# Performance work log

Hardware: AMD Instinct MI355X
Metric: run time of the kernel (lower is better)

## Reference

```python
import jax, jax.numpy as jnp
import numpy as np

B, P, C = 32, 8732, 21
TOP_K = 200
CONF_THRESH = 0.01
NMS_THRESH = 0.45
VAR0, VAR1 = 0.1, 0.2  # VOC PRIOR_BOX VARIANCE


def setup_inputs() -> dict:
    key = jax.random.key(0)
    k1, k2, k3 = jax.random.split(key, 3)
    loc_data = jax.random.normal(k1, (B, P, 4), jnp.float32)
    conf_data = jax.random.uniform(k2, (B, P, C), jnp.float32)
    prior_data = jax.random.uniform(k3, (P, 4), jnp.float32)
    return {"loc_data": loc_data, "conf_data": conf_data, "prior_data": prior_data}


def _decode(loc, priors):
    # priors are (cx, cy, w, h); returns (x1, y1, x2, y2)
    cxcy = priors[:, :2] + loc[:, :2] * VAR0 * priors[:, 2:]
    wh = priors[:, 2:] * jnp.exp(loc[:, 2:] * VAR1)
    x1y1 = cxcy - wh * 0.5
    return jnp.concatenate([x1y1, x1y1 + wh], axis=1)  # [P,4]


def _nms_class(boxes, scores):
    # boxes [P,4], scores [P] -> [TOP_K,5] rows of (score, x1, y1, x2, y2)
    s = jnp.where(scores > CONF_THRESH, scores, -1.0)
    top_s, idx = jax.lax.top_k(s, TOP_K)          # descending scores
    b = boxes[idx]                                 # [K,4]
    valid = top_s > CONF_THRESH
    x1, y1, x2, y2 = b[:, 0], b[:, 1], b[:, 2], b[:, 3]
    area = (x2 - x1) * (y2 - y1)
    # pairwise intersection / IoU [K,K]
    xx1 = jnp.maximum(x1[:, None], x1[None, :])
    yy1 = jnp.maximum(y1[:, None], y1[None, :])
    xx2 = jnp.minimum(x2[:, None], x2[None, :])
    yy2 = jnp.minimum(y2[:, None], y2[None, :])
    inter = jnp.clip(xx2 - xx1, 0.0) * jnp.clip(yy2 - yy1, 0.0)
    union = area[:, None] + area[None, :] - inter
    iou = inter / union
    ar = jnp.arange(TOP_K)

    def step(carry, j):
        kept, suppressed = carry
        is_kept = valid[j] & ~suppressed[j]
        kept = kept.at[j].set(is_kept)
        suppressed = suppressed | (is_kept & (iou[j] > NMS_THRESH) & (ar > j))
        return (kept, suppressed), None

    (kept, _), _ = jax.lax.scan(
        step, (jnp.zeros(TOP_K, bool), jnp.zeros(TOP_K, bool)), ar)
    # compact kept rows to the front (matches output[i, cl, :count] = ...)
    pos = jnp.cumsum(kept) - 1
    safe = jnp.where(kept, pos, TOP_K)
    rows = jnp.concatenate([top_s[:, None], b], axis=1)  # [K,5]
    out = jnp.zeros((TOP_K + 1, 5), rows.dtype).at[safe].set(rows)[:TOP_K]
    return out


def reference(loc_data, conf_data, prior_data):
    def per_image(loc, conf):
        boxes = _decode(loc, prior_data)           # [P,4]
        return jax.vmap(lambda s: _nms_class(boxes, s), in_axes=1)(conf)  # [C,K,5]

    out = jax.vmap(per_image)(loc_data, conf_data)  # [B,C,K,5]
    return out.at[:, 0].set(0.0)  # class 0 (background) is skipped in original
```

## Files before the change

### kernel.cpp

```cpp
#include <hip/hip_runtime.h>
#include <stdint.h>

#define B_ 32
#define P_ 8732
#define PPAD 8736
#define C_ 21
#define TOPK 200
#define CONF_T 0.01f
#define NMS_T 0.45f
#define NCH2 35
#define NT 512
#define KV4 5

__device__ __forceinline__ uint32_t f2s(float f) {
    uint32_t u = __float_as_uint(f);
    return (u & 0x80000000u) ? ~u : (u | 0x80000000u);
}
__device__ __forceinline__ float s2f(uint32_t s) {
    uint32_t b = (s & 0x80000000u) ? (s & 0x7FFFFFFFu) : ~s;
    return __uint_as_float(b);
}

__global__ __launch_bounds__(256) void transpose_keys(const float* __restrict__ conf,
                                                      uint32_t* __restrict__ keys) {
    const int b = blockIdx.x / NCH2;
    const int ch = blockIdx.x % NCH2;
    const int p0 = ch * 256;
    const int n = min(256, P_ - p0);
    const int tid = threadIdx.x;
    __shared__ float tile[256 * C_];
    const float* src = conf + ((size_t)b * P_ + p0) * C_;
    const int tot = n * C_;
    for (int i = tid; i < tot; i += 256) tile[i] = src[i];
    __syncthreads();
    uint32_t* dst = keys + (size_t)b * C_ * PPAD + p0;
    if (tid < n) {
        #pragma unroll
        for (int c = 0; c < C_; ++c) {
            float v = tile[tid * C_ + c];
            v = (v > CONF_T) ? v : -1.0f;
            dst[(size_t)c * PPAD + tid] = f2s(v);
        }
    }
    if (ch == NCH2 - 1 && tid >= n && tid < n + (PPAD - P_)) {
        #pragma unroll
        for (int c = 0; c < C_; ++c) dst[(size_t)c * PPAD + tid] = 0u;
    }
}

template<bool RAW>
__global__ __launch_bounds__(NT, 6) void detect_kernel(
    const float* __restrict__ loc, const float* __restrict__ prior,
    const uint32_t* __restrict__ keys, const float* __restrict__ conf,
    float* __restrict__ out)
{
    const int task = blockIdx.x;
    const int b = task / C_;
    const int c = task % C_;
    const int tid = threadIdx.x;
    const int lane = tid & 63;
    float* outp = out + (size_t)task * TOPK * 5;

    if (c == 0) {
        for (int e = tid; e < TOPK * 5; e += NT) outp[e] = 0.0f;
        return;
    }

    __shared__ uint32_t hist[256];
    __shared__ uint32_t wtot[4];
    __shared__ uint64_t cand[256];
    __shared__ float4 bbox[TOPK];
    __shared__ float bar[TOPK], bs[TOPK];
    __shared__ unsigned long long msk[TOPK * 4];
    __shared__ unsigned long long vmask[4];
    __shared__ int order[TOPK];
    __shared__ int s_cnt, s_nk, s_flags;
    __shared__ uint32_t s_pref, s_want;

    uint4 kv[KV4];
    if (!RAW) {
        const uint4* kp = (const uint4*)(keys + (size_t)task * PPAD);
        #pragma unroll
        for (int r = 0; r < KV4; ++r) {
            int q = tid + r * NT;
            kv[r] = (q < PPAD / 4) ? kp[q] : make_uint4(0u, 0u, 0u, 0u);
        }
    } else {
        const float* sp = conf + (size_t)b * P_ * C_ + c;
        #pragma unroll
        for (int r = 0; r < KV4; ++r) {
            uint32_t uu[4];
            #pragma unroll
            for (int c4 = 0; c4 < 4; ++c4) {
                int p = (tid + r * NT) * 4 + c4;
                if (p < P_) {
                    float v = sp[(size_t)p * C_];
                    v = (v > CONF_T) ? v : -1.0f;
                    uu[c4] = f2s(v);
                } else uu[c4] = 0u;
            }
            kv[r] = make_uint4(uu[0], uu[1], uu[2], uu[3]);
        }
    }

    uint32_t pref = 0, want = TOPK;
    for (int level = 3; level >= 0; --level) {
        const int shift = level * 8;
        const uint32_t himask = (level == 3) ? 0u : (0xFFFFFFFFu << (shift + 8));
        if (tid < 256) hist[tid] = 0;
        __syncthreads();
        if (level == 3) {
            auto agg = [&](uint32_t u) {
                uint32_t bin = u >> 24;
                unsigned long long rem = __ballot(1);
                while (rem) {
                    int src = __ffsll(rem) - 1;
                    uint32_t bref = __shfl(bin, src);
                    unsigned long long same = __ballot(bin == bref) & rem;
                    if (lane == src) atomicAdd(&hist[bref], (uint32_t)__popcll(same));
                    rem &= ~same;
                }
            };
            #pragma unroll
            for (int r = 0; r < KV4; ++r) {
                agg(kv[r].x); agg(kv[r].y); agg(kv[r].z); agg(kv[r].w);
            }
        } else {
            auto one = [&](uint32_t u) {
                if ((u & himask) == pref) atomicAdd(&hist[(u >> shift) & 0xFFu], 1u);
            };
            #pragma unroll
            for (int r = 0; r < KV4; ++r) {
                one(kv[r].x); one(kv[r].y); one(kv[r].z); one(kv[r].w);
            }
        }
        __syncthreads();
        uint32_t h = 0, I = 0;
        if (tid < 256) {
            h = hist[tid];
            I = h;
            #pragma unroll
            for (int d = 1; d < 64; d <<= 1) {
                uint32_t v = __shfl_down(I, d);
                if (lane + d < 64) I += v;
            }
            if (lane == 0) wtot[tid >> 6] = I;
        }
        __syncthreads();
        if (tid < 256) {
            uint32_t off = 0;
            for (int w2 = (tid >> 6) + 1; w2 < 4; ++w2) off += wtot[w2];
            I += off;
            uint32_t E = I - h;
            if (I >= want && E < want) {
                s_pref = pref | ((uint32_t)tid << shift);
                s_want = want - E;
                s_flags = ((TOPK - want) + I <= 256) ? 1 : 0;
            }
        }
        __syncthreads();
        pref = s_pref; want = s_want;
        int done = s_flags;
        __syncthreads();
        if (done) break;
    }
    const uint32_t vthr = pref;

    if (tid == 0) s_cnt = 0;
    __syncthreads();
    #pragma unroll
    for (int r = 0; r < KV4; ++r) {
        const int pb = (tid + r * NT) * 4;
        uint32_t uu[4] = {kv[r].x, kv[r].y, kv[r].z, kv[r].w};
        #pragma unroll
        for (int c4 = 0; c4 < 4; ++c4) {
            uint32_t u = uu[c4];
            if (u >= vthr) {
                int pos = atomicAdd(&s_cnt, 1);
                if (pos < 256) cand[pos] = ((uint64_t)u << 32) | (uint32_t)(~(uint32_t)(pb + c4));
            }
        }
    }
    __syncthreads();
    if (tid < 256 && tid >= s_cnt) cand[tid] = 0ull;
    __syncthreads();

    uint64_t v = (tid < 256) ? cand[tid] : 0ull;
    for (int kk = 2; kk <= 256; kk <<= 1) {
        for (int j = kk >> 1; j > 0; j >>= 1) {
            if (j >= 64) {
                __syncthreads();
                if (tid < 256) cand[tid] = v;
                __syncthreads();
                if (tid < 256) {
                    uint64_t pv = cand[tid ^ j];
                    bool keepmax = (((tid & j) == 0) == ((tid & kk) == 0));
                    v = keepmax ? (v > pv ? v : pv) : (v < pv ? v : pv);
                }
            } else if (tid < 256) {
                uint64_t pv = __shfl_xor(v, j);
                bool keepmax = (((tid & j) == 0) == ((tid & kk) == 0));
                v = keepmax ? (v > pv ? v : pv) : (v < pv ? v : pv);
            }
        }
    }

    float my_sc = -1.0f;
    if (tid < TOPK) {
        uint32_t su = (uint32_t)(v >> 32);
        int p = (int)(~(uint32_t)v);
        my_sc = s2f(su);
        const float4 l4 = *(const float4*)(loc + ((size_t)b * P_ + p) * 4);
        const float4 pr = *(const float4*)(prior + (size_t)p * 4);
        float cx = __fadd_rn(pr.x, __fmul_rn(__fmul_rn(l4.x, 0.1f), pr.z));
        float cy = __fadd_rn(pr.y, __fmul_rn(__fmul_rn(l4.y, 0.1f), pr.w));
        float ew = (float)exp((double)__fmul_rn(l4.z, 0.2f));
        float eh = (float)exp((double)__fmul_rn(l4.w, 0.2f));
        float w  = __fmul_rn(pr.z, ew);
        float h  = __fmul_rn(pr.w, eh);
        float x1 = __fsub_rn(cx, __fmul_rn(w, 0.5f));
        float y1 = __fsub_rn(cy, __fmul_rn(h, 0.5f));
        float x2 = __fadd_rn(x1, w);
        float y2 = __fadd_rn(y1, h);
        bs[tid] = my_sc;
        bbox[tid] = make_float4(x1, y1, x2, y2);
        bar[tid] = __fmul_rn(__fsub_rn(x2, x1), __fsub_rn(y2, y1));
    }
    for (int i2 = tid; i2 < TOPK * 4; i2 += NT) msk[i2] = 0ull;
    {
        unsigned long long bm = __ballot(tid < TOPK && my_sc > CONF_T);
        if (lane == 0 && tid < 256) vmask[tid >> 6] = bm;
    }
    __syncthreads();

    if (tid < 500) {
        const int rp = tid / 5;
        const int s  = tid - rp * 5;
        #pragma unroll
        for (int pass = 0; pass < 2; ++pass) {
            const int j  = pass ? (199 - rp) : rp;
            const int i0 = pass ? (200 - rp + s) : (rp + 1 + s);
            const float4 bj = bbox[j];
            const float  aj = bar[j];
            for (int i = i0; i < TOPK; i += 5) {
                const float4 bi = bbox[i];
                float xx1 = fmaxf(bj.x, bi.x);
                float yy1 = fmaxf(bj.y, bi.y);
                float xx2 = fminf(bj.z, bi.z);
                float yy2 = fminf(bj.w, bi.w);
                float dx = fmaxf(__fsub_rn(xx2, xx1), 0.0f);
                float dy = fmaxf(__fsub_rn(yy2, yy1), 0.0f);
                float inter = __fmul_rn(dx, dy);
                if (inter > 0.0f) {
                    float uni = __fsub_rn(__fadd_rn(aj, bar[i]), inter);
                    float t45 = __fmul_rn(NMS_T, uni);
                    float mar = __fmul_rn(t45, 1e-6f);
                    bool sup;
                    if (inter > __fadd_rn(t45, mar)) sup = true;
                    else if (inter < __fsub_rn(t45, mar)) sup = false;
                    else sup = (inter / uni > NMS_T);
                    if (sup) atomicOr(&msk[j * 4 + (i >> 6)], 1ull << (i & 63));
                }
            }
        }
    }
    __syncthreads();

    if (tid < 64) {
        const int L = tid;
        unsigned long long s0 = 0, s1 = 0, s2 = 0, s3 = 0;
        const unsigned long long vm0 = vmask[0], vm1 = vmask[1],
                                 vm2 = vmask[2], vm3 = vmask[3];
        int nk = 0;
        #pragma unroll
        for (int w = 0; w < 4; ++w) {
            const int j = (w << 6) | L;
            unsigned long long r0 = 0, r1 = 0, r2 = 0, r3 = 0;
            if (j < TOPK) {
                const unsigned long long* mr = &msk[j * 4];
                r0 = mr[0]; r1 = mr[1]; r2 = mr[2]; r3 = mr[3];
            }
            const unsigned long long vw = (w == 0) ? vm0 : (w == 1) ? vm1
                                        : (w == 2) ? vm2 : vm3;
            const unsigned long long sw = (w == 0) ? s0 : (w == 1) ? s1
                                        : (w == 2) ? s2 : s3;
            unsigned long long alive = vw & ~sw;
            while (alive) {
                int jl = __ffsll(alive) - 1;
                if (L == 0) order[nk] = (w << 6) | jl;
                ++nk;
                s0 |= __shfl(r0, jl); s1 |= __shfl(r1, jl);
                s2 |= __shfl(r2, jl); s3 |= __shfl(r3, jl);
                const unsigned long long swn = (w == 0) ? s0 : (w == 1) ? s1
                                             : (w == 2) ? s2 : s3;
                alive &= ~swn;
                alive &= ~(1ull << jl);
            }
        }
        if (L == 0) s_nk = nk;
    }
    __syncthreads();

    const int nk = s_nk;
    for (int e = tid; e < TOPK * 5; e += NT) {
        int r = e / 5;
        int f = e - r * 5;
        float val = 0.0f;
        if (r < nk) {
            int j = order[r];
            float4 bb = bbox[j];
            val = (f == 0) ? bs[j] : (f == 1) ? bb.x : (f == 2) ? bb.y
                : (f == 3) ? bb.z : bb.w;
        }
        outp[e] = val;
    }
}

extern "C" void kernel_launch(void* const* d_in, const int* in_sizes, int n_in,
                              void* d_out, int out_size, void* d_ws, size_t ws_size,
                              hipStream_t stream) {
    const float* loc   = (const float*)d_in[0];
    const float* conf  = (const float*)d_in[1];
    const float* prior = (const float*)d_in[2];
    float* out = (float*)d_out;

    const size_t need = (size_t)B_ * C_ * PPAD * sizeof(uint32_t);
    if (ws_size >= need) {
        uint32_t* keys = (uint32_t*)d_ws;
        transpose_keys<<<B_ * NCH2, 256, 0, stream>>>(conf, keys);
        detect_kernel<false><<<B_ * C_, NT, 0, stream>>>(loc, prior, keys, conf, out);
    } else {
        detect_kernel<true><<<B_ * C_, NT, 0, stream>>>(loc, prior, nullptr, conf, out);
    }
}
```

Measured before the change: 138.4 us.

## Pack four NMS tasks per block and replace radix histogram with 2-bit threshold search

Each 1024-thread block now processes four (image, class) tasks with 256 threads each, instead of one task per 512-thread block. The 8-bit atomic-histogram radix select is replaced by a search that fixes two bits per round, counting keys above three candidate thresholds with per-thread compares and a packed wave reduction. The pairwise IoU work is redistributed over two lanes per row. This is meant to remove shared-memory atomic contention and idle threads, but it adds more select rounds, block-wide syncs shared across the four tasks, and more registers per thread (nine uint4 keys).

```diff
diff --git a/kernel.cpp b/kernel.cpp
--- a/kernel.cpp
+++ b/kernel.cpp
@@ -9,8 +9,12 @@
 #define CONF_T 0.01f
 #define NMS_T 0.45f
 #define NCH2 35
-#define NT 512
-#define KV4 5
+#define GT 4
+#define TT 256
+#define NTB (GT * TT)
+#define KV4 9
+#define NTASK (B_ * C_)
+#define NBLK (NTASK / GT)
 
 __device__ __forceinline__ uint32_t f2s(float f) {
     uint32_t u = __float_as_uint(f);
@@ -49,41 +53,38 @@
 }
 
 template<bool RAW>
-__global__ __launch_bounds__(NT, 6) void detect_kernel(
+__global__ __launch_bounds__(NTB, 4) void detect_kernel(
     const float* __restrict__ loc, const float* __restrict__ prior,
     const uint32_t* __restrict__ keys, const float* __restrict__ conf,
     float* __restrict__ out)
 {
-    const int task = blockIdx.x;
+    const int tid  = threadIdx.x;
+    const int sub  = tid >> 8;
+    const int tt   = tid & 255;
+    const int lane = tid & 63;
+    const int wv   = (tid >> 6) & 3;
+    const int task = blockIdx.x * GT + sub;
     const int b = task / C_;
     const int c = task % C_;
-    const int tid = threadIdx.x;
-    const int lane = tid & 63;
     float* outp = out + (size_t)task * TOPK * 5;
 
-    if (c == 0) {
-        for (int e = tid; e < TOPK * 5; e += NT) outp[e] = 0.0f;
-        return;
-    }
-
-    __shared__ uint32_t hist[256];
-    __shared__ uint32_t wtot[4];
-    __shared__ uint64_t cand[256];
-    __shared__ float4 bbox[TOPK];
-    __shared__ float bar[TOPK], bs[TOPK];
-    __shared__ unsigned long long msk[TOPK * 4];
-    __shared__ unsigned long long vmask[4];
-    __shared__ int order[TOPK];
-    __shared__ int s_cnt, s_nk, s_flags;
-    __shared__ uint32_t s_pref, s_want;
+    __shared__ uint64_t cand[GT][256];
+    __shared__ float4 bbox[GT][TOPK];
+    __shared__ float bar[GT][TOPK], bs[GT][TOPK];
+    __shared__ unsigned long long msk[GT][TOPK * 4];
+    __shared__ unsigned long long vmask[GT][4];
+    __shared__ int order[GT][TOPK];
+    __shared__ int s_cnt[GT], s_nk[GT];
+    __shared__ uint64_t warr[GT][4];
+    __shared__ uint32_t s_donemask;
 
     uint4 kv[KV4];
     if (!RAW) {
         const uint4* kp = (const uint4*)(keys + (size_t)task * PPAD);
         #pragma unroll
         for (int r = 0; r < KV4; ++r) {
-            int q = tid + r * NT;
-            kv[r] = (q < PPAD / 4) ? kp[q] : make_uint4(0u, 0u, 0u, 0u);
+            int q = tt + r * TT;
+            kv[r] = (c != 0 && q < PPAD / 4) ? kp[q] : make_uint4(0u, 0u, 0u, 0u);
         }
     } else {
         const float* sp = conf + (size_t)b * P_ * C_ + c;
@@ -91,122 +92,114 @@
         for (int r = 0; r < KV4; ++r) {
             uint32_t uu[4];
             #pragma unroll
-            for (int c4 = 0; c4 < 4; ++c4) {
-                int p = (tid + r * NT) * 4 + c4;
-                if (p < P_) {
+            for (int q = 0; q < 4; ++q) {
+                int p = (tt + r * TT) * 4 + q;
+                if (c != 0 && p < P_) {
                     float v = sp[(size_t)p * C_];
                     v = (v > CONF_T) ? v : -1.0f;
-                    uu[c4] = f2s(v);
-                } else uu[c4] = 0u;
+                    uu[q] = f2s(v);
+                } else uu[q] = 0u;
             }
             kv[r] = make_uint4(uu[0], uu[1], uu[2], uu[3]);
         }
     }
 
-    uint32_t pref = 0, want = TOPK;
-    for (int level = 3; level >= 0; --level) {
-        const int shift = level * 8;
-        const uint32_t himask = (level == 3) ? 0u : (0xFFFFFFFFu << (shift + 8));
-        if (tid < 256) hist[tid] = 0;
-        __syncthreads();
-        if (level == 3) {
-            auto agg = [&](uint32_t u) {
-                uint32_t bin = u >> 24;
-                unsigned long long rem = __ballot(1);
-                while (rem) {
-                    int src = __ffsll(rem) - 1;
-                    uint32_t bref = __shfl(bin, src);
-                    unsigned long long same = __ballot(bin == bref) & rem;
-                    if (lane == src) atomicAdd(&hist[bref], (uint32_t)__popcll(same));
-                    rem &= ~same;
-                }
-            };
+    if (tid == 0) s_donemask = 0;
+    if (tt == 0) s_cnt[sub] = 0;
+    __syncthreads();
+    if (c == 0 && tt == 0) atomicOr(&s_donemask, 1u << sub);
+    __syncthreads();
+
+    uint32_t pref = 0, cprev = KV4 * TT * 4;
+    int bp = 30;
+    bool done = (c == 0);
+    while (s_donemask != 0xFu) {
+        if (!done) {
+            const uint32_t tA = pref | (1u << bp);
+            const uint32_t tB = pref | (2u << bp);
+            const uint32_t tC = pref | (3u << bp);
+            uint32_t cA = 0, cB = 0, cC = 0;
             #pragma unroll
             for (int r = 0; r < KV4; ++r) {
-                agg(kv[r].x); agg(kv[r].y); agg(kv[r].z); agg(kv[r].w);
-            }
-        } else {
-            auto one = [&](uint32_t u) {
-                if ((u & himask) == pref) atomicAdd(&hist[(u >> shift) & 0xFFu], 1u);
-            };
+                const uint32_t uu[4] = {kv[r].x, kv[r].y, kv[r].z, kv[r].w};
+                #pragma unroll
+                for (int q = 0; q < 4; ++q) {
+                    const uint32_t u = uu[q];
+                    cA += (u >= tA); cB += (u >= tB); cC += (u >= tC);
+                }
+            }
+            unsigned long long pk = (unsigned long long)cA
+                                  | ((unsigned long long)cB << 21)
+                                  | ((unsigned long long)cC << 42);
             #pragma unroll
-            for (int r = 0; r < KV4; ++r) {
-                one(kv[r].x); one(kv[r].y); one(kv[r].z); one(kv[r].w);
-            }
+            for (int d = 1; d < 64; d <<= 1) pk += __shfl_down(pk, d);
+            if (lane == 0) warr[sub][wv] = pk;
         }
         __syncthreads();
-        uint32_t h = 0, I = 0;
-        if (tid < 256) {
-            h = hist[tid];
-            I = h;
+        if (!done) {
+            const unsigned long long tot = warr[sub][0] + warr[sub][1]
+                                         + warr[sub][2] + warr[sub][3];
+            const uint32_t M = (1u << 21) - 1;
+            const uint32_t cA = (uint32_t)tot & M;
+            const uint32_t cB = (uint32_t)(tot >> 21) & M;
+            const uint32_t cC = (uint32_t)(tot >> 42) & M;
+            uint32_t cNew;
+            if      (cC >= TOPK) { pref |= (3u << bp); cNew = cC; }
+            else if (cB >= TOPK) { pref |= (2u << bp); cNew = cB; }
+            else if (cA >= TOPK) { pref |= (1u << bp); cNew = cA; }
+            else                 { cNew = cprev; }
+            cprev = cNew;
+            bp -= 2;
+            if (cNew <= 256 || bp < 0) {
+                done = true;
+                if (tt == 0) atomicOr(&s_donemask, 1u << sub);
+            }
+        }
+        __syncthreads();
+    }
+    const uint32_t vthr = pref;
+
+    if (c != 0) {
+        #pragma unroll
+        for (int r = 0; r < KV4; ++r) {
+            const int pb = (tt + r * TT) * 4;
+            const uint32_t uu[4] = {kv[r].x, kv[r].y, kv[r].z, kv[r].w};
             #pragma unroll
-            for (int d = 1; d < 64; d <<= 1) {
-                uint32_t v = __shfl_down(I, d);
-                if (lane + d < 64) I += v;
-            }
-            if (lane == 0) wtot[tid >> 6] = I;
-        }
-        __syncthreads();
-        if (tid < 256) {
-            uint32_t off = 0;
-            for (int w2 = (tid >> 6) + 1; w2 < 4; ++w2) off += wtot[w2];
-            I += off;
-            uint32_t E = I - h;
-            if (I >= want && E < want) {
-                s_pref = pref | ((uint32_t)tid << shift);
-                s_want = want - E;
-                s_flags = ((TOPK - want) + I <= 256) ? 1 : 0;
-            }
-        }
-        __syncthreads();
-        pref = s_pref; want = s_want;
-        int done = s_flags;
-        __syncthreads();
-        if (done) break;
-    }
-    const uint32_t vthr = pref;
-
-    if (tid == 0) s_cnt = 0;
-    __syncthreads();
-    #pragma unroll
-    for (int r = 0; r < KV4; ++r) {
-        const int pb = (tid + r * NT) * 4;
-        uint32_t uu[4] = {kv[r].x, kv[r].y, kv[r].z, kv[r].w};
-        #pragma unroll
-        for (int c4 = 0; c4 < 4; ++c4) {
-            uint32_t u = uu[c4];
-            if (u >= vthr) {
-                int pos = atomicAdd(&s_cnt, 1);
-                if (pos < 256) cand[pos] = ((uint64_t)u << 32) | (uint32_t)(~(uint32_t)(pb + c4));
-            }
-        }
-    }
-    __syncthreads();
-    if (tid < 256 && tid >= s_cnt) cand[tid] = 0ull;
-    __syncthreads();
-
-    uint64_t v = (tid < 256) ? cand[tid] : 0ull;
+            for (int q = 0; q < 4; ++q) {
+                const uint32_t u = uu[q];
+                if (u >= vthr) {
+                    int pos = atomicAdd(&s_cnt[sub], 1);
+                    if (pos < 256) cand[sub][pos] = ((uint64_t)u << 32)
+                                                  | (uint32_t)(~(uint32_t)(pb + q));
+                }
+            }
+        }
+    }
+    __syncthreads();
+    if (tt >= s_cnt[sub]) cand[sub][tt] = 0ull;
+    for (int i2 = tt; i2 < TOPK * 4; i2 += TT) msk[sub][i2] = 0ull;
+    __syncthreads();
+
+    uint64_t v = cand[sub][tt];
     for (int kk = 2; kk <= 256; kk <<= 1) {
         for (int j = kk >> 1; j > 0; j >>= 1) {
             if (j >= 64) {
                 __syncthreads();
-                if (tid < 256) cand[tid] = v;
+                cand[sub][tt] = v;
                 __syncthreads();
-                if (tid < 256) {
-                    uint64_t pv = cand[tid ^ j];
-                    bool keepmax = (((tid & j) == 0) == ((tid & kk) == 0));
-                    v = keepmax ? (v > pv ? v : pv) : (v < pv ? v : pv);
-                }
-            } else if (tid < 256) {
+                uint64_t pv = cand[sub][tt ^ j];
+                bool keepmax = (((tt & j) == 0) == ((tt & kk) == 0));
+                v = keepmax ? (v > pv ? v : pv) : (v < pv ? v : pv);
+            } else {
                 uint64_t pv = __shfl_xor(v, j);
-                bool keepmax = (((tid & j) == 0) == ((tid & kk) == 0));
+                bool keepmax = (((tt & j) == 0) == ((tt & kk) == 0));
                 v = keepmax ? (v > pv ? v : pv) : (v < pv ? v : pv);
             }
         }
     }
 
     float my_sc = -1.0f;
-    if (tid < TOPK) {
+    if (c != 0 && tt < TOPK) {
         uint32_t su = (uint32_t)(v >> 32);
         int p = (int)(~(uint32_t)v);
         my_sc = s2f(su);
@@ -222,28 +215,27 @@
         float y1 = __fsub_rn(cy, __fmul_rn(h, 0.5f));
         float x2 = __fadd_rn(x1, w);
         float y2 = __fadd_rn(y1, h);
-        bs[tid] = my_sc;
-        bbox[tid] = make_float4(x1, y1, x2, y2);
-        bar[tid] = __fmul_rn(__fsub_rn(x2, x1), __fsub_rn(y2, y1));
-    }
-    for (int i2 = tid; i2 < TOPK * 4; i2 += NT) msk[i2] = 0ull;
+        bs[sub][tt] = my_sc;
+        bbox[sub][tt] = make_float4(x1, y1, x2, y2);
+        bar[sub][tt] = __fmul_rn(__fsub_rn(x2, x1), __fsub_rn(y2, y1));
+    }
     {
-        unsigned long long bm = __ballot(tid < TOPK && my_sc > CONF_T);
-        if (lane == 0 && tid < 256) vmask[tid >> 6] = bm;
-    }
-    __syncthreads();
-
-    if (tid < 500) {
-        const int rp = tid / 5;
-        const int s  = tid - rp * 5;
+        unsigned long long bm = __ballot(tt < TOPK && my_sc > CONF_T);
+        if (lane == 0) vmask[sub][wv] = bm;
+    }
+    __syncthreads();
+
+    if (c != 0 && tt < 2 * (TOPK / 2)) {
+        const int rp = tt >> 1;
+        const int s  = tt & 1;
         #pragma unroll
         for (int pass = 0; pass < 2; ++pass) {
             const int j  = pass ? (199 - rp) : rp;
-            const int i0 = pass ? (200 - rp + s) : (rp + 1 + s);
-            const float4 bj = bbox[j];
-            const float  aj = bar[j];
-            for (int i = i0; i < TOPK; i += 5) {
-                const float4 bi = bbox[i];
+            const int i0 = j + 1 + s;
+            const float4 bj = bbox[sub][j];
+            const float  aj = bar[sub][j];
+            for (int i = i0; i < TOPK; i += 2) {
+                const float4 bi = bbox[sub][i];
                 float xx1 = fmaxf(bj.x, bi.x);
                 float yy1 = fmaxf(bj.y, bi.y);
                 float xx2 = fminf(bj.z, bi.z);
@@ -252,32 +244,32 @@
                 float dy = fmaxf(__fsub_rn(yy2, yy1), 0.0f);
                 float inter = __fmul_rn(dx, dy);
                 if (inter > 0.0f) {
-                    float uni = __fsub_rn(__fadd_rn(aj, bar[i]), inter);
+                    float uni = __fsub_rn(__fadd_rn(aj, bar[sub][i]), inter);
                     float t45 = __fmul_rn(NMS_T, uni);
                     float mar = __fmul_rn(t45, 1e-6f);
                     bool sup;
                     if (inter > __fadd_rn(t45, mar)) sup = true;
                     else if (inter < __fsub_rn(t45, mar)) sup = false;
                     else sup = (inter / uni > NMS_T);
-                    if (sup) atomicOr(&msk[j * 4 + (i >> 6)], 1ull << (i & 63));
+                    if (sup) atomicOr(&msk[sub][j * 4 + (i >> 6)], 1ull << (i & 63));
                 }
             }
         }
     }
     __syncthreads();
 
-    if (tid < 64) {
-        const int L = tid;
+    if (tt < 64) {
+        const int L = tt;
         unsigned long long s0 = 0, s1 = 0, s2 = 0, s3 = 0;
-        const unsigned long long vm0 = vmask[0], vm1 = vmask[1],
-                                 vm2 = vmask[2], vm3 = vmask[3];
+        const unsigned long long vm0 = vmask[sub][0], vm1 = vmask[sub][1],
+                                 vm2 = vmask[sub][2], vm3 = vmask[sub][3];
         int nk = 0;
         #pragma unroll
         for (int w = 0; w < 4; ++w) {
             const int j = (w << 6) | L;
             unsigned long long r0 = 0, r1 = 0, r2 = 0, r3 = 0;
             if (j < TOPK) {
-                const unsigned long long* mr = &msk[j * 4];
+                const unsigned long long* mr = &msk[sub][j * 4];
                 r0 = mr[0]; r1 = mr[1]; r2 = mr[2]; r3 = mr[3];
             }
             const unsigned long long vw = (w == 0) ? vm0 : (w == 1) ? vm1
@@ -287,7 +279,7 @@
             unsigned long long alive = vw & ~sw;
             while (alive) {
                 int jl = __ffsll(alive) - 1;
-                if (L == 0) order[nk] = (w << 6) | jl;
+                if (L == 0) order[sub][nk] = (w << 6) | jl;
                 ++nk;
                 s0 |= __shfl(r0, jl); s1 |= __shfl(r1, jl);
                 s2 |= __shfl(r2, jl); s3 |= __shfl(r3, jl);
@@ -297,19 +289,19 @@
                 alive &= ~(1ull << jl);
             }
         }
-        if (L == 0) s_nk = nk;
-    }
-    __syncthreads();
-
-    const int nk = s_nk;
-    for (int e = tid; e < TOPK * 5; e += NT) {
+        if (L == 0) s_nk[sub] = nk;
+    }
+    __syncthreads();
+
+    const int nk = (c != 0) ? s_nk[sub] : 0;
+    for (int e = tt; e < TOPK * 5; e += TT) {
         int r = e / 5;
         int f = e - r * 5;
         float val = 0.0f;
         if (r < nk) {
-            int j = order[r];
-            float4 bb = bbox[j];
-            val = (f == 0) ? bs[j] : (f == 1) ? bb.x : (f == 2) ? bb.y
+            int j = order[sub][r];
+            float4 bb = bbox[sub][j];
+            val = (f == 0) ? bs[sub][j] : (f == 1) ? bb.x : (f == 2) ? bb.y
                 : (f == 3) ? bb.z : bb.w;
         }
         outp[e] = val;
@@ -328,8 +320,8 @@
     if (ws_size >= need) {
         uint32_t* keys = (uint32_t*)d_ws;
         transpose_keys<<<B_ * NCH2, 256, 0, stream>>>(conf, keys);
-        detect_kernel<false><<<B_ * C_, NT, 0, stream>>>(loc, prior, keys, conf, out);
+        detect_kernel<false><<<NBLK, NTB, 0, stream>>>(loc, prior, keys, conf, out);
     } else {
-        detect_kernel<true><<<B_ * C_, NT, 0, stream>>>(loc, prior, nullptr, conf, out);
-    }
-}
+        detect_kernel<true><<<NBLK, NTB, 0, stream>>>(loc, prior, nullptr, conf, out);
+    }
+}
```

Result: slower. 167.3 us (+20.9%).

## Cut barriers in radix select and batch NMS suppression propagation

Applied to the files above, without the earlier changes.

Double-buffers the histogram so clearing it needs no extra barrier on the first levels, and has each thread scan four bins at once, which removes the cross-wave prefix step and its barrier. Zeroing of the suppression mask and of the counter moves before the select loop, which drops further barriers. In the serial NMS walk, only the current 64-bit word is updated per kept box. Suppression of later words is applied afterwards with one OR-reduction across the wave, so fewer shuffles sit on the serial chain. The scan is more complex, and the early-out now depends on reading shared flags without a trailing barrier.

```diff
diff --git a/kernel.cpp b/kernel.cpp
--- a/kernel.cpp
+++ b/kernel.cpp
@@ -66,8 +66,7 @@
         return;
     }
 
-    __shared__ uint32_t hist[256];
-    __shared__ uint32_t wtot[4];
+    __shared__ uint32_t hist[512];
     __shared__ uint64_t cand[256];
     __shared__ float4 bbox[TOPK];
     __shared__ float bar[TOPK], bs[TOPK];
@@ -103,12 +102,19 @@
         }
     }
 
+    if (tid == 0) s_cnt = 0;
+    if (tid < 512) hist[tid] = 0;
+    for (int i2 = tid; i2 < TOPK * 4; i2 += NT) msk[i2] = 0ull;
+    __syncthreads();
+
     uint32_t pref = 0, want = TOPK;
     for (int level = 3; level >= 0; --level) {
         const int shift = level * 8;
-        const uint32_t himask = (level == 3) ? 0u : (0xFFFFFFFFu << (shift + 8));
-        if (tid < 256) hist[tid] = 0;
-        __syncthreads();
+        uint32_t* H = hist + ((((3 - level) & 1)) << 8);
+        if (level <= 1) {
+            if (tid < 256) H[tid] = 0;
+            __syncthreads();
+        }
         if (level == 3) {
             auto agg = [&](uint32_t u) {
                 uint32_t bin = u >> 24;
@@ -117,7 +123,7 @@
                     int src = __ffsll(rem) - 1;
                     uint32_t bref = __shfl(bin, src);
                     unsigned long long same = __ballot(bin == bref) & rem;
-                    if (lane == src) atomicAdd(&hist[bref], (uint32_t)__popcll(same));
+                    if (lane == src) atomicAdd(&H[bref], (uint32_t)__popcll(same));
                     rem &= ~same;
                 }
             };
@@ -126,8 +132,9 @@
                 agg(kv[r].x); agg(kv[r].y); agg(kv[r].z); agg(kv[r].w);
             }
         } else {
+            const uint32_t himask = 0xFFFFFFFFu << (shift + 8);
             auto one = [&](uint32_t u) {
-                if ((u & himask) == pref) atomicAdd(&hist[(u >> shift) & 0xFFu], 1u);
+                if ((u & himask) == pref) atomicAdd(&H[(u >> shift) & 0xFFu], 1u);
             };
             #pragma unroll
             for (int r = 0; r < KV4; ++r) {
@@ -135,39 +142,44 @@
             }
         }
         __syncthreads();
-        uint32_t h = 0, I = 0;
-        if (tid < 256) {
-            h = hist[tid];
-            I = h;
+        if (tid < 64) {
+            uint4 bb = ((const uint4*)H)[tid];
+            uint32_t s = bb.x + bb.y + bb.z + bb.w;
+            uint32_t I = s;
             #pragma unroll
             for (int d = 1; d < 64; d <<= 1) {
-                uint32_t v = __shfl_down(I, d);
-                if (lane + d < 64) I += v;
-            }
-            if (lane == 0) wtot[tid >> 6] = I;
-        }
-        __syncthreads();
-        if (tid < 256) {
-            uint32_t off = 0;
-            for (int w2 = (tid >> 6) + 1; w2 < 4; ++w2) off += wtot[w2];
-            I += off;
-            uint32_t E = I - h;
-            if (I >= want && E < want) {
-                s_pref = pref | ((uint32_t)tid << shift);
-                s_want = want - E;
-                s_flags = ((TOPK - want) + I <= 256) ? 1 : 0;
+                uint32_t t2 = __shfl_down(I, d);
+                if (lane + d < 64) I += t2;
+            }
+            const uint32_t above = I - s;
+            const uint32_t e3 = above,      i3 = above + bb.w;
+            const uint32_t e2 = i3,         i2 = i3 + bb.z;
+            const uint32_t e1 = i2,         i1 = i2 + bb.y;
+            const uint32_t e0 = i1,         i0 = i1 + bb.x;
+            const uint32_t base = (uint32_t)TOPK - want;
+            if (i3 >= want && e3 < want) {
+                s_pref = pref | ((uint32_t)(4 * tid + 3) << shift);
+                s_want = want - e3; s_flags = (base + i3 <= 256);
+            }
+            if (i2 >= want && e2 < want) {
+                s_pref = pref | ((uint32_t)(4 * tid + 2) << shift);
+                s_want = want - e2; s_flags = (base + i2 <= 256);
+            }
+            if (i1 >= want && e1 < want) {
+                s_pref = pref | ((uint32_t)(4 * tid + 1) << shift);
+                s_want = want - e1; s_flags = (base + i1 <= 256);
+            }
+            if (i0 >= want && e0 < want) {
+                s_pref = pref | ((uint32_t)(4 * tid + 0) << shift);
+                s_want = want - e0; s_flags = (base + i0 <= 256);
             }
         }
         __syncthreads();
         pref = s_pref; want = s_want;
-        int done = s_flags;
-        __syncthreads();
-        if (done) break;
+        if (s_flags) break;
     }
     const uint32_t vthr = pref;
 
-    if (tid == 0) s_cnt = 0;
-    __syncthreads();
     #pragma unroll
     for (int r = 0; r < KV4; ++r) {
         const int pb = (tid + r * NT) * 4;
@@ -226,7 +238,6 @@
         bbox[tid] = make_float4(x1, y1, x2, y2);
         bar[tid] = __fmul_rn(__fsub_rn(x2, x1), __fsub_rn(y2, y1));
     }
-    for (int i2 = tid; i2 < TOPK * 4; i2 += NT) msk[i2] = 0ull;
     {
         unsigned long long bm = __ballot(tid < TOPK && my_sc > CONF_T);
         if (lane == 0 && tid < 256) vmask[tid >> 6] = bm;
@@ -268,9 +279,12 @@
 
     if (tid < 64) {
         const int L = tid;
-        unsigned long long s0 = 0, s1 = 0, s2 = 0, s3 = 0;
-        const unsigned long long vm0 = vmask[0], vm1 = vmask[1],
-                                 vm2 = vmask[2], vm3 = vmask[3];
+        auto or_reduce = [&](unsigned long long x) {
+            #pragma unroll
+            for (int d = 1; d < 64; d <<= 1) x |= __shfl_xor(x, d);
+            return x;
+        };
+        unsigned long long s1 = 0, s2 = 0, s3 = 0;
         int nk = 0;
         #pragma unroll
         for (int w = 0; w < 4; ++w) {
@@ -280,21 +294,32 @@
                 const unsigned long long* mr = &msk[j * 4];
                 r0 = mr[0]; r1 = mr[1]; r2 = mr[2]; r3 = mr[3];
             }
-            const unsigned long long vw = (w == 0) ? vm0 : (w == 1) ? vm1
-                                        : (w == 2) ? vm2 : vm3;
-            const unsigned long long sw = (w == 0) ? s0 : (w == 1) ? s1
-                                        : (w == 2) ? s2 : s3;
-            unsigned long long alive = vw & ~sw;
+            const unsigned long long rself = (w == 0) ? r0 : (w == 1) ? r1
+                                           : (w == 2) ? r2 : r3;
+            unsigned long long sw = (w == 0) ? 0ull : (w == 1) ? s1
+                                  : (w == 2) ? s2 : s3;
+            unsigned long long alive = vmask[w] & ~sw;
+            unsigned long long pm = 0;
             while (alive) {
                 int jl = __ffsll(alive) - 1;
                 if (L == 0) order[nk] = (w << 6) | jl;
                 ++nk;
-                s0 |= __shfl(r0, jl); s1 |= __shfl(r1, jl);
-                s2 |= __shfl(r2, jl); s3 |= __shfl(r3, jl);
-                const unsigned long long swn = (w == 0) ? s0 : (w == 1) ? s1
-                                             : (w == 2) ? s2 : s3;
-                alive &= ~swn;
-                alive &= ~(1ull << jl);
+                sw |= __shfl(rself, jl);
+                pm |= (1ull << jl);
+                alive &= ~(sw | (1ull << jl));
+            }
+            if (pm) {
+                const bool picked = (pm >> L) & 1ull;
+                if (w == 0) {
+                    s1 |= or_reduce(picked ? r1 : 0ull);
+                    s2 |= or_reduce(picked ? r2 : 0ull);
+                    s3 |= or_reduce(picked ? r3 : 0ull);
+                } else if (w == 1) {
+                    s2 |= or_reduce(picked ? r2 : 0ull);
+                    s3 |= or_reduce(picked ? r3 : 0ull);
+                } else if (w == 2) {
+                    s3 |= or_reduce(picked ? r3 : 0ull);
+                }
             }
         }
         if (L == 0) s_nk = nk;
```

Result: no change. 136.3 us (-1.5%).
